# Kernel tuning notes

Measured on AMD Instinct MI355X. Metric: run time of the kernel, lower is better.

## Reference

```python
import jax, jax.numpy as jnp
import numpy as np
import math

# ---- module hyperparams (from init_kwargs) ----
L = 10            # number of hash-grid levels
DIM = 4           # features per level
LOG2T = 16
T = 1 << LOG2T    # hash table size per level
BASE = 16         # base resolution
PLS = 2.0         # per_level_scale
SCALE_MULTI = 0.5
HID = 64
IN_DIM = L * DIM  # 40
OUT_DIM = 13      # 1 + 12
N = 1_000_000

# growth factor b = exp((ln(finest) - ln(base)) / (L - 1)), finest = base * pls**L
B_GROWTH = math.exp((math.log(BASE * PLS ** L) - math.log(BASE)) / (L - 1))
RES = [int(math.floor(BASE * B_GROWTH ** l)) for l in range(L)]

PRIMES = np.array([1, 2654435761, 805459861], dtype=np.uint32)
# 8 corner offsets of a voxel
OFFS = np.array([[i, j, k] for i in (0, 1) for j in (0, 1) for k in (0, 1)], dtype=np.uint32)


def _hash_coords(c):
    # c: uint32 [N, 8, 3] -> int32 [N, 8] indices into table of size T
    p = jnp.asarray(PRIMES)
    h = (c[..., 0] * p[0]) ^ (c[..., 1] * p[1]) ^ (c[..., 2] * p[2])
    return (h & jnp.uint32(T - 1)).astype(jnp.int32)


def _encode(x, tables):
    # x: [N,3] in [0,1]; tables: [L, T, DIM] -> [N, DIM, L]
    offs_u = jnp.asarray(OFFS)                      # uint32 [8,3]
    offs_b = jnp.asarray(OFFS.astype(bool))         # bool   [8,3]
    feats = []
    for l in range(L):
        xs = x * RES[l]
        bottom = jnp.floor(xs)
        frac = xs - bottom                          # [N,3]
        corners = bottom.astype(jnp.uint32)[:, None, :] + offs_u[None]  # [N,8,3]
        idx = _hash_coords(corners)                 # [N,8]
        cf = tables[l][idx]                         # [N,8,DIM] gather
        # trilinear weights: prod over dims of frac (if offset==1) else (1-frac)
        w = jnp.prod(jnp.where(offs_b[None], frac[:, None, :], 1.0 - frac[:, None, :]), axis=-1)  # [N,8]
        feats.append(jnp.einsum('nc,ncd->nd', w, cf))  # [N,DIM]
    return jnp.stack(feats, axis=-1)                # [N, DIM, L]


def setup_inputs() -> dict:
    key = jax.random.key(0)
    ks = jax.random.split(key, 10)
    x = jax.random.uniform(ks[0], (N, 3), dtype=jnp.float32)
    cr = jax.random.uniform(ks[1], (N,), dtype=jnp.float32)
    tables = jax.random.uniform(ks[2], (L, T, DIM), dtype=jnp.float32, minval=-1e-4, maxval=1e-4)
    gain = math.sqrt(2.0)  # calculate_gain('relu')

    def xavier(k, fan_in, fan_out):
        a = gain * math.sqrt(6.0 / (fan_in + fan_out))
        return jax.random.uniform(k, (fan_in, fan_out), dtype=jnp.float32, minval=-a, maxval=a)

    W1 = xavier(ks[3], IN_DIM, HID)
    b1 = jnp.zeros((HID,), jnp.float32)
    W2 = xavier(ks[4], HID, HID)
    b2 = jnp.zeros((HID,), jnp.float32)
    W3 = xavier(ks[5], HID, OUT_DIM)
    b3 = jnp.zeros((OUT_DIM,), jnp.float32)
    return {"x": x, "cr": cr, "tables": tables,
            "W1": W1, "b1": b1, "W2": W2, "b2": b2, "W3": W3, "b3": b3}


def reference(x, cr, tables, W1, b1, W2, b2, W3, b3):
    enc = _encode(x, tables)                        # [N, DIM, L]
    cr_s = cr.reshape(-1) * SCALE_MULTI             # [N]
    n = jnp.arange(L, dtype=jnp.float32).reshape(1, 1, L)
    denom = PLS * 4.0 * n * cr_s[:, None, None]     # [N,1,L]
    erf_x = 1.0 / jnp.sqrt(jnp.maximum(denom, 1e-12))  # safe_div/safe_sqrt; erf(huge)=1 at n=0
    scaling = jax.lax.erf(erf_x)
    h = (enc * scaling).reshape(-1, IN_DIM)         # [N, 40]
    h = jax.nn.selu(h @ W1 + b1)
    h = jax.nn.selu(h @ W2 + b2)
    return h @ W3 + b3                              # [N, 13]
```

## Files before the change

### kernel.cpp

```cpp
#include <hip/hip_runtime.h>
#include <cmath>

typedef unsigned int uint32;
typedef __bf16 bf16;
typedef __bf16 bf16x8 __attribute__((ext_vector_type(8)));
typedef float f32x4 __attribute__((ext_vector_type(4)));

#define LVLS 10
#define TSIZE 65536
#define TMASK 65535u
#define PRIME2 2654435761u
#define PRIME3 805459861u

#define WOFF_W1 0
#define WOFF_W2 4096
#define WOFF_W3 8192
#define W_ELEMS 9216
#define DQ_OFF 18432
#define SC_OFF 18496
#define TAB_OFF_B 18560
#define TAB_ELEMS_F (LVLS * TSIZE * 4)
#define WS_NEEDED ((size_t)TAB_OFF_B + (size_t)TAB_ELEMS_F)

struct KParams { float resf[LVLS]; };

__global__ void scale_kernel(const float* __restrict__ tables, unsigned* __restrict__ scales) {
  int tid = blockIdx.x * 256 + threadIdx.x;
  int i4 = tid * 4;
  if (i4 >= TAB_ELEMS_F) return;
  float4 v = *(const float4*)(tables + i4);
  float m = fmaxf(fmaxf(fabsf(v.x), fabsf(v.y)), fmaxf(fabsf(v.z), fabsf(v.w)));
#pragma unroll
  for (int off = 32; off; off >>= 1) m = fmaxf(m, __shfl_xor(m, off, 64));
  if ((threadIdx.x & 63) == 0) {
    int l = i4 >> 18;
    atomicMax(scales + l, __float_as_uint(m));
  }
}

__global__ void quant_kernel(const float* __restrict__ W1, const float* __restrict__ W2,
                             const float* __restrict__ W3, const float* __restrict__ tables,
                             char* __restrict__ ws8, int do_tab) {
  int tid = blockIdx.x * 256 + threadIdx.x;
  bf16* wsb = (bf16*)ws8;
  if (tid < W_ELEMS) {
    float v;
    if (tid < 4096) {
      int n = tid >> 6, k = tid & 63;
      v = (k < 40) ? W1[k * 64 + n] : 0.f;
    } else if (tid < 8192) {
      int t2 = tid - 4096; int n = t2 >> 6, k = t2 & 63;
      v = W2[k * 64 + n];
    } else {
      int t3 = tid - 8192; int n = t3 >> 6, k = t3 & 63;
      v = (n < 13) ? W3[k * 13 + n] : 0.f;
    }
    wsb[tid] = (bf16)v;
  }
  const unsigned* scales = (const unsigned*)(ws8 + SC_OFF);
  if (tid < LVLS) {
    float s = __uint_as_float(scales[tid]);
    ((float*)(ws8 + DQ_OFF))[tid] = s * (1.0f / 127.0f);
  }
  if (do_tab) {
    int i4 = tid * 4;
    if (i4 < TAB_ELEMS_F) {
      float4 v = *(const float4*)(tables + i4);
      int l = i4 >> 18;
      float s = __uint_as_float(scales[l]);
      float r = (s > 0.f) ? 127.f / s : 0.f;
      int q0 = (int)rintf(fminf(fmaxf(v.x * r, -127.f), 127.f));
      int q1 = (int)rintf(fminf(fmaxf(v.y * r, -127.f), 127.f));
      int q2 = (int)rintf(fminf(fmaxf(v.z * r, -127.f), 127.f));
      int q3 = (int)rintf(fminf(fmaxf(v.w * r, -127.f), 127.f));
      unsigned p = (q0 & 0xff) | ((q1 & 0xff) << 8) | ((q2 & 0xff) << 16) | ((q3 & 0xff) << 24);
      *(unsigned*)(ws8 + TAB_OFF_B + i4) = p;
    }
  }
}

__device__ __forceinline__ float selu_f(float v) {
  float neg = 1.6732632423543772f * (__expf(v) - 1.0f);
  return 1.0507009873554805f * (v > 0.f ? v : neg);
}

__device__ __forceinline__ void gemm_stage(const bf16* __restrict__ Arow,
                                           const bf16* __restrict__ Bbase,
                                           const float* __restrict__ bvec,
                                           bf16* __restrict__ Hwr, int lr) {
  float bias[4];
#pragma unroll
  for (int nt = 0; nt < 4; ++nt) bias[nt] = bvec[nt * 16 + lr];
  f32x4 acc[4][4];
#pragma unroll
  for (int ms = 0; ms < 4; ++ms)
#pragma unroll
    for (int nt = 0; nt < 4; ++nt) {
      f32x4 a = {bias[nt], bias[nt], bias[nt], bias[nt]};
      acc[ms][nt] = a;
    }
  bf16x8 Bf[2][4];
#pragma unroll
  for (int ks = 0; ks < 2; ++ks)
#pragma unroll
    for (int nt = 0; nt < 4; ++nt)
      Bf[ks][nt] = *(const bf16x8*)(Bbase + nt * 1024 + ks * 32);
#pragma unroll
  for (int ks = 0; ks < 2; ++ks) {
    bf16x8 Af[4];
#pragma unroll
    for (int ms = 0; ms < 4; ++ms) Af[ms] = *(const bf16x8*)(Arow + ms * 1152 + ks * 32);
#pragma unroll
    for (int ms = 0; ms < 4; ++ms)
#pragma unroll
      for (int nt = 0; nt < 4; ++nt)
        acc[ms][nt] = __builtin_amdgcn_mfma_f32_16x16x32_bf16(Af[ms], Bf[ks][nt], acc[ms][nt], 0, 0, 0);
  }
#pragma unroll
  for (int ms = 0; ms < 4; ++ms)
#pragma unroll
    for (int nt = 0; nt < 4; ++nt)
#pragma unroll
      for (int r = 0; r < 4; ++r)
        Hwr[(ms * 16 + r) * 72 + nt * 16 + lr] = (bf16)selu_f(acc[ms][nt][r]);
}

template <bool TB>
__global__ __launch_bounds__(256, 4)
void ngp_fused(const float* __restrict__ x, const float* __restrict__ cr,
               const float* __restrict__ tables, const char* __restrict__ ws8,
               const float* __restrict__ b1, const float* __restrict__ b2,
               const float* __restrict__ b3, float* __restrict__ out,
               int N, KParams kp) {
  __shared__ bf16 Hbuf[256 * 72];
  const int tid = threadIdx.x;
  const int n = blockIdx.x * 256 + tid;
  const int ncl = (n < N) ? n : 0;

  const float px = x[ncl * 3 + 0];
  const float py = x[ncl * 3 + 1];
  const float pz = x[ncl * 3 + 2];
  const float crv = cr[ncl];
  const float* dq = (const float*)(ws8 + DQ_OFF);

  float feat[40];
#pragma unroll
  for (int l = 0; l < LVLS; ++l) {
    const float rs = kp.resf[l];
    float xs = px * rs, ys = py * rs, zs = pz * rs;
    float bx = floorf(xs), by = floorf(ys), bz = floorf(zs);
    float fx = xs - bx, fy = ys - by, fz = zs - bz;
    uint32 cx = (uint32)bx, cy = (uint32)by, cz = (uint32)bz;
    uint32 hx0 = cx, hx1 = cx + 1u;
    uint32 hy0 = cy * PRIME2, hy1 = hy0 + PRIME2;
    uint32 hz0 = cz * PRIME3, hz1 = hz0 + PRIME3;
    uint32 idx[8];
    idx[0] = (hx0 ^ hy0 ^ hz0) & TMASK; idx[1] = (hx0 ^ hy0 ^ hz1) & TMASK;
    idx[2] = (hx0 ^ hy1 ^ hz0) & TMASK; idx[3] = (hx0 ^ hy1 ^ hz1) & TMASK;
    idx[4] = (hx1 ^ hy0 ^ hz0) & TMASK; idx[5] = (hx1 ^ hy0 ^ hz1) & TMASK;
    idx[6] = (hx1 ^ hy1 ^ hz0) & TMASK; idx[7] = (hx1 ^ hy1 ^ hz1) & TMASK;

    float f[8][4];
    if (TB) {
      const unsigned* tb = ((const unsigned*)(ws8 + TAB_OFF_B)) + l * TSIZE;
#pragma unroll
      for (int c = 0; c < 8; ++c) {
        unsigned q = tb[idx[c]];
        f[c][0] = (float)(signed char)(q & 0xff);
        f[c][1] = (float)(signed char)((q >> 8) & 0xff);
        f[c][2] = (float)(signed char)((q >> 16) & 0xff);
        f[c][3] = (float)(signed char)(q >> 24);
      }
    } else {
      const float4* tb = ((const float4*)tables) + l * TSIZE;
#pragma unroll
      for (int c = 0; c < 8; ++c) {
        float4 q = tb[idx[c]];
        f[c][0] = q.x; f[c][1] = q.y; f[c][2] = q.z; f[c][3] = q.w;
      }
    }
    float wx1 = fx, wx0 = 1.f - fx, wy1 = fy, wy0 = 1.f - fy, wz1 = fz, wz0 = 1.f - fz;
    float wxy00 = wx0 * wy0, wxy01 = wx0 * wy1, wxy10 = wx1 * wy0, wxy11 = wx1 * wy1;
    float w[8] = {wxy00 * wz0, wxy00 * wz1, wxy01 * wz0, wxy01 * wz1,
                  wxy10 * wz0, wxy10 * wz1, wxy11 * wz0, wxy11 * wz1};
    float a0 = 0.f, a1 = 0.f, a2 = 0.f, a3 = 0.f;
#pragma unroll
    for (int c = 0; c < 8; ++c) {
      a0 = fmaf(w[c], f[c][0], a0);
      a1 = fmaf(w[c], f[c][1], a1);
      a2 = fmaf(w[c], f[c][2], a2);
      a3 = fmaf(w[c], f[c][3], a3);
    }
    float s = erff(rsqrtf(fmaxf(4.0f * (float)l * crv, 1e-12f)));
    if (TB) s *= dq[l];
    feat[0 * 10 + l] = a0 * s;
    feat[1 * 10 + l] = a1 * s;
    feat[2 * 10 + l] = a2 * s;
    feat[3 * 10 + l] = a3 * s;
  }

  {
    bf16* row = Hbuf + tid * 72;
#pragma unroll
    for (int c = 0; c < 5; ++c) {
      bf16x8 v;
#pragma unroll
      for (int j = 0; j < 8; ++j) v[j] = (bf16)feat[c * 8 + j];
      *(bf16x8*)(row + c * 8) = v;
    }
    bf16x8 z;
#pragma unroll
    for (int j = 0; j < 8; ++j) z[j] = (bf16)0.f;
    *(bf16x8*)(row + 40) = z;
    *(bf16x8*)(row + 48) = z;
    *(bf16x8*)(row + 56) = z;
  }
  __syncthreads();

  const int w = tid >> 6;
  const int lane = tid & 63;
  const int lr = lane & 15;
  const int quad = lane >> 4;
  const bf16* wsb = (const bf16*)ws8;

  const bf16* Arow = Hbuf + (w * 64 + lr) * 72 + quad * 8;
  bf16* Hwr = Hbuf + (w * 64 + quad * 4) * 72;

  gemm_stage(Arow, wsb + WOFF_W1 + lr * 64 + quad * 8, b1, Hwr, lr);
  __syncthreads();
  gemm_stage(Arow, wsb + WOFF_W2 + lr * 64 + quad * 8, b2, Hwr, lr);
  __syncthreads();

  {
    float b3v = (lr < 13) ? b3[lr] : 0.f;
    f32x4 acc3[4];
#pragma unroll
    for (int ms = 0; ms < 4; ++ms) {
      f32x4 a = {b3v, b3v, b3v, b3v};
      acc3[ms] = a;
    }
    const bf16* B3b = wsb + WOFF_W3 + lr * 64 + quad * 8;
    bf16x8 B3[2];
    B3[0] = *(const bf16x8*)(B3b);
    B3[1] = *(const bf16x8*)(B3b + 32);
#pragma unroll
    for (int ks = 0; ks < 2; ++ks) {
      bf16x8 Af[4];
#pragma unroll
      for (int ms = 0; ms < 4; ++ms) Af[ms] = *(const bf16x8*)(Arow + ms * 1152 + ks * 32);
#pragma unroll
      for (int ms = 0; ms < 4; ++ms)
        acc3[ms] = __builtin_amdgcn_mfma_f32_16x16x32_bf16(Af[ms], B3[ks], acc3[ms], 0, 0, 0);
    }
    const int rbase = blockIdx.x * 256 + w * 64 + quad * 4;
#pragma unroll
    for (int ms = 0; ms < 4; ++ms)
#pragma unroll
      for (int r = 0; r < 4; ++r) {
        int rowg = rbase + ms * 16 + r;
        if (lr < 13 && rowg < N) out[rowg * 13 + lr] = acc3[ms][r];
      }
  }
}

extern "C" void kernel_launch(void* const* d_in, const int* in_sizes, int n_in,
                              void* d_out, int out_size, void* d_ws, size_t ws_size,
                              hipStream_t stream) {
  const float* x      = (const float*)d_in[0];
  const float* cr     = (const float*)d_in[1];
  const float* tables = (const float*)d_in[2];
  const float* W1     = (const float*)d_in[3];
  const float* b1     = (const float*)d_in[4];
  const float* W2     = (const float*)d_in[5];
  const float* b2     = (const float*)d_in[6];
  const float* W3     = (const float*)d_in[7];
  const float* b3     = (const float*)d_in[8];
  float* out = (float*)d_out;
  const int N = in_sizes[1];

  KParams kp;
  double B = exp((log(16.0 * pow(2.0, 10.0)) - log(16.0)) / 9.0);
  for (int l = 0; l < LVLS; ++l) kp.resf[l] = (float)floor(16.0 * pow(B, (double)l));

  char* ws8 = (char*)d_ws;
  const bool tb = ws_size >= WS_NEEDED;

  const int qblocks = (TAB_ELEMS_F / 4 + 255) / 256;
  if (tb) {
    hipMemsetAsync(ws8 + SC_OFF, 0, 64, stream);
    scale_kernel<<<qblocks, 256, 0, stream>>>(tables, (unsigned*)(ws8 + SC_OFF));
    quant_kernel<<<qblocks, 256, 0, stream>>>(W1, W2, W3, tables, ws8, 1);
  } else {
    quant_kernel<<<(W_ELEMS + 255) / 256, 256, 0, stream>>>(W1, W2, W3, tables, ws8, 0);
  }

  int blocks = (N + 255) / 256;
  if (tb)
    ngp_fused<true><<<blocks, 256, 0, stream>>>(x, cr, tables, ws8, b1, b2, b3, out, N, kp);
  else
    ngp_fused<false><<<blocks, 256, 0, stream>>>(x, cr, tables, ws8, b1, b2, b3, out, N, kp);
}
```

Measured before the change: 485.1 us.

## Swizzle LDS activations, prefetch next-level gathers, stage output for coalesced stores

Several changes land together. The LDS activation buffer drops its 72-element padded rows for a 64-element XOR-swizzled layout, and the GEMM stage now loads all A fragments once and processes the N-tiles in two halves to cut register pressure. Launch bounds go from 4 to 5 waves per SIMD. The int8 table path is software-pipelined: level l+1 gathers are issued before level l is consumed. Table values are stored with a +128 offset so unpacking is a plain unsigned convert, with the offset subtracted after accumulation, and level-0 erf is skipped. Output rows are staged in LDS and written as coalesced float4 stores. The risks are more live registers from the prefetch under the tighter launch bound, and extra barriers.

```diff
diff --git a/kernel.cpp b/kernel.cpp
--- a/kernel.cpp
+++ b/kernel.cpp
@@ -69,10 +69,10 @@
       int l = i4 >> 18;
       float s = __uint_as_float(scales[l]);
       float r = (s > 0.f) ? 127.f / s : 0.f;
-      int q0 = (int)rintf(fminf(fmaxf(v.x * r, -127.f), 127.f));
-      int q1 = (int)rintf(fminf(fmaxf(v.y * r, -127.f), 127.f));
-      int q2 = (int)rintf(fminf(fmaxf(v.z * r, -127.f), 127.f));
-      int q3 = (int)rintf(fminf(fmaxf(v.w * r, -127.f), 127.f));
+      int q0 = (int)rintf(fminf(fmaxf(v.x * r, -127.f), 127.f)) + 128;
+      int q1 = (int)rintf(fminf(fmaxf(v.y * r, -127.f), 127.f)) + 128;
+      int q2 = (int)rintf(fminf(fmaxf(v.z * r, -127.f), 127.f)) + 128;
+      int q3 = (int)rintf(fminf(fmaxf(v.w * r, -127.f), 127.f)) + 128;
       unsigned p = (q0 & 0xff) | ((q1 & 0xff) << 8) | ((q2 & 0xff) << 16) | ((q3 & 0xff) << 24);
       *(unsigned*)(ws8 + TAB_OFF_B + i4) = p;
     }
@@ -84,55 +84,82 @@
   return 1.0507009873554805f * (v > 0.f ? v : neg);
 }
 
-__device__ __forceinline__ void gemm_stage(const bf16* __restrict__ Arow,
+__device__ __forceinline__ bf16* hswz(bf16* Hb, int row, int cb) {
+  return (bf16*)((char*)Hb + (row << 7) + (cb ^ ((row & 7) << 4)));
+}
+
+__device__ __forceinline__ void gemm_stage(bf16* __restrict__ Hb, int w, int lr, int quad,
                                            const bf16* __restrict__ Bbase,
-                                           const float* __restrict__ bvec,
-                                           bf16* __restrict__ Hwr, int lr) {
-  float bias[4];
-#pragma unroll
-  for (int nt = 0; nt < 4; ++nt) bias[nt] = bvec[nt * 16 + lr];
-  f32x4 acc[4][4];
-#pragma unroll
-  for (int ms = 0; ms < 4; ++ms)
-#pragma unroll
-    for (int nt = 0; nt < 4; ++nt) {
-      f32x4 a = {bias[nt], bias[nt], bias[nt], bias[nt]};
-      acc[ms][nt] = a;
-    }
-  bf16x8 Bf[2][4];
+                                           const float* __restrict__ bvec) {
+  bf16x8 Af[2][4];
 #pragma unroll
   for (int ks = 0; ks < 2; ++ks)
 #pragma unroll
-    for (int nt = 0; nt < 4; ++nt)
-      Bf[ks][nt] = *(const bf16x8*)(Bbase + nt * 1024 + ks * 32);
-#pragma unroll
-  for (int ks = 0; ks < 2; ++ks) {
-    bf16x8 Af[4];
-#pragma unroll
-    for (int ms = 0; ms < 4; ++ms) Af[ms] = *(const bf16x8*)(Arow + ms * 1152 + ks * 32);
-#pragma unroll
     for (int ms = 0; ms < 4; ++ms)
-#pragma unroll
-      for (int nt = 0; nt < 4; ++nt)
-        acc[ms][nt] = __builtin_amdgcn_mfma_f32_16x16x32_bf16(Af[ms], Bf[ks][nt], acc[ms][nt], 0, 0, 0);
-  }
-#pragma unroll
-  for (int ms = 0; ms < 4; ++ms)
-#pragma unroll
-    for (int nt = 0; nt < 4; ++nt)
-#pragma unroll
-      for (int r = 0; r < 4; ++r)
-        Hwr[(ms * 16 + r) * 72 + nt * 16 + lr] = (bf16)selu_f(acc[ms][nt][r]);
-}
+      Af[ks][ms] = *(const bf16x8*)hswz(Hb, w * 64 + ms * 16 + lr, quad * 16 + ks * 64);
+#pragma unroll
+  for (int h = 0; h < 2; ++h) {
+    f32x4 acc[4][2];
+#pragma unroll
+    for (int nt2 = 0; nt2 < 2; ++nt2) {
+      float b = bvec[(h * 2 + nt2) * 16 + lr];
+#pragma unroll
+      for (int ms = 0; ms < 4; ++ms) {
+        f32x4 a = {b, b, b, b};
+        acc[ms][nt2] = a;
+      }
+    }
+#pragma unroll
+    for (int ks = 0; ks < 2; ++ks) {
+      bf16x8 B0 = *(const bf16x8*)(Bbase + (h * 2 + 0) * 1024 + ks * 32);
+      bf16x8 B1 = *(const bf16x8*)(Bbase + (h * 2 + 1) * 1024 + ks * 32);
+#pragma unroll
+      for (int ms = 0; ms < 4; ++ms) {
+        acc[ms][0] = __builtin_amdgcn_mfma_f32_16x16x32_bf16(Af[ks][ms], B0, acc[ms][0], 0, 0, 0);
+        acc[ms][1] = __builtin_amdgcn_mfma_f32_16x16x32_bf16(Af[ks][ms], B1, acc[ms][1], 0, 0, 0);
+      }
+    }
+#pragma unroll
+    for (int ms = 0; ms < 4; ++ms)
+#pragma unroll
+      for (int nt2 = 0; nt2 < 2; ++nt2)
+#pragma unroll
+        for (int r = 0; r < 4; ++r) {
+          int row = w * 64 + quad * 4 + ms * 16 + r;
+          *hswz(Hb, row, ((h * 2 + nt2) * 16 + lr) * 2) = (bf16)selu_f(acc[ms][nt2][r]);
+        }
+  }
+}
+
+#define CALC_IDX(L, IDX, F0, F1, F2)                                   \
+  do {                                                                 \
+    const float rs_ = kp.resf[(L)];                                    \
+    float xs_ = px * rs_, ys_ = py * rs_, zs_ = pz * rs_;              \
+    float bx_ = floorf(xs_), by_ = floorf(ys_), bz_ = floorf(zs_);     \
+    (F0) = xs_ - bx_; (F1) = ys_ - by_; (F2) = zs_ - bz_;              \
+    uint32 cx_ = (uint32)bx_, cy_ = (uint32)by_, cz_ = (uint32)bz_;    \
+    uint32 hy0_ = cy_ * PRIME2, hy1_ = hy0_ + PRIME2;                  \
+    uint32 hz0_ = cz_ * PRIME3, hz1_ = hz0_ + PRIME3;                  \
+    uint32 cx1_ = cx_ + 1u;                                            \
+    uint32 bse_ = (uint32)(L) << 16;                                   \
+    (IDX)[0] = ((cx_ ^ hy0_ ^ hz0_) & TMASK) | bse_;                   \
+    (IDX)[1] = ((cx_ ^ hy0_ ^ hz1_) & TMASK) | bse_;                   \
+    (IDX)[2] = ((cx_ ^ hy1_ ^ hz0_) & TMASK) | bse_;                   \
+    (IDX)[3] = ((cx_ ^ hy1_ ^ hz1_) & TMASK) | bse_;                   \
+    (IDX)[4] = ((cx1_ ^ hy0_ ^ hz0_) & TMASK) | bse_;                  \
+    (IDX)[5] = ((cx1_ ^ hy0_ ^ hz1_) & TMASK) | bse_;                  \
+    (IDX)[6] = ((cx1_ ^ hy1_ ^ hz0_) & TMASK) | bse_;                  \
+    (IDX)[7] = ((cx1_ ^ hy1_ ^ hz1_) & TMASK) | bse_;                  \
+  } while (0)
 
 template <bool TB>
-__global__ __launch_bounds__(256, 4)
+__global__ __launch_bounds__(256, 5)
 void ngp_fused(const float* __restrict__ x, const float* __restrict__ cr,
                const float* __restrict__ tables, const char* __restrict__ ws8,
                const float* __restrict__ b1, const float* __restrict__ b2,
                const float* __restrict__ b3, float* __restrict__ out,
                int N, KParams kp) {
-  __shared__ bf16 Hbuf[256 * 72];
+  __shared__ __align__(16) bf16 Hbuf[256 * 64];
   const int tid = threadIdx.x;
   const int n = blockIdx.x * 256 + tid;
   const int ncl = (n < N) ? n : 0;
@@ -144,76 +171,102 @@
   const float* dq = (const float*)(ws8 + DQ_OFF);
 
   float feat[40];
-#pragma unroll
-  for (int l = 0; l < LVLS; ++l) {
-    const float rs = kp.resf[l];
-    float xs = px * rs, ys = py * rs, zs = pz * rs;
-    float bx = floorf(xs), by = floorf(ys), bz = floorf(zs);
-    float fx = xs - bx, fy = ys - by, fz = zs - bz;
-    uint32 cx = (uint32)bx, cy = (uint32)by, cz = (uint32)bz;
-    uint32 hx0 = cx, hx1 = cx + 1u;
-    uint32 hy0 = cy * PRIME2, hy1 = hy0 + PRIME2;
-    uint32 hz0 = cz * PRIME3, hz1 = hz0 + PRIME3;
-    uint32 idx[8];
-    idx[0] = (hx0 ^ hy0 ^ hz0) & TMASK; idx[1] = (hx0 ^ hy0 ^ hz1) & TMASK;
-    idx[2] = (hx0 ^ hy1 ^ hz0) & TMASK; idx[3] = (hx0 ^ hy1 ^ hz1) & TMASK;
-    idx[4] = (hx1 ^ hy0 ^ hz0) & TMASK; idx[5] = (hx1 ^ hy0 ^ hz1) & TMASK;
-    idx[6] = (hx1 ^ hy1 ^ hz0) & TMASK; idx[7] = (hx1 ^ hy1 ^ hz1) & TMASK;
-
-    float f[8][4];
-    if (TB) {
-      const unsigned* tb = ((const unsigned*)(ws8 + TAB_OFF_B)) + l * TSIZE;
+
+  if constexpr (TB) {
+    const unsigned* tb = (const unsigned*)(ws8 + TAB_OFF_B);
+    uint32 idx0[8];
+    float pf0, pf1, pf2;
+    CALC_IDX(0, idx0, pf0, pf1, pf2);
+    unsigned qP[8];
+#pragma unroll
+    for (int c = 0; c < 8; ++c) qP[c] = tb[idx0[c]];
+#pragma unroll
+    for (int l = 0; l < LVLS; ++l) {
+      unsigned qN[8];
+      float nf0 = 0.f, nf1 = 0.f, nf2 = 0.f;
+      if (l + 1 < LVLS) {
+        uint32 idxN[8];
+        CALC_IDX(l + 1, idxN, nf0, nf1, nf2);
+#pragma unroll
+        for (int c = 0; c < 8; ++c) qN[c] = tb[idxN[c]];
+      }
+      float fx = pf0, fy = pf1, fz = pf2;
+      float wx1 = fx, wx0 = 1.f - fx, wy1 = fy, wy0 = 1.f - fy, wz1 = fz, wz0 = 1.f - fz;
+      float wxy00 = wx0 * wy0, wxy01 = wx0 * wy1, wxy10 = wx1 * wy0, wxy11 = wx1 * wy1;
+      float w8[8] = {wxy00 * wz0, wxy00 * wz1, wxy01 * wz0, wxy01 * wz1,
+                     wxy10 * wz0, wxy10 * wz1, wxy11 * wz0, wxy11 * wz1};
+      float a0 = 0.f, a1 = 0.f, a2 = 0.f, a3 = 0.f;
 #pragma unroll
       for (int c = 0; c < 8; ++c) {
-        unsigned q = tb[idx[c]];
-        f[c][0] = (float)(signed char)(q & 0xff);
-        f[c][1] = (float)(signed char)((q >> 8) & 0xff);
-        f[c][2] = (float)(signed char)((q >> 16) & 0xff);
-        f[c][3] = (float)(signed char)(q >> 24);
-      }
-    } else {
-      const float4* tb = ((const float4*)tables) + l * TSIZE;
+        unsigned q = qP[c];
+        float u0 = (float)(q & 0xffu);
+        float u1 = (float)((q >> 8) & 0xffu);
+        float u2 = (float)((q >> 16) & 0xffu);
+        float u3 = (float)(q >> 24);
+        a0 = fmaf(w8[c], u0, a0);
+        a1 = fmaf(w8[c], u1, a1);
+        a2 = fmaf(w8[c], u2, a2);
+        a3 = fmaf(w8[c], u3, a3);
+      }
+      float s = (l == 0) ? dq[0]
+                         : erff(rsqrtf(fmaxf(4.0f * (float)l * crv, 1e-12f))) * dq[l];
+      feat[0 * 10 + l] = (a0 - 128.f) * s;
+      feat[1 * 10 + l] = (a1 - 128.f) * s;
+      feat[2 * 10 + l] = (a2 - 128.f) * s;
+      feat[3 * 10 + l] = (a3 - 128.f) * s;
+      if (l + 1 < LVLS) {
+#pragma unroll
+        for (int c = 0; c < 8; ++c) qP[c] = qN[c];
+        pf0 = nf0; pf1 = nf1; pf2 = nf2;
+      }
+    }
+  } else {
+#pragma unroll
+    for (int l = 0; l < LVLS; ++l) {
+      uint32 idx[8];
+      float fx, fy, fz;
+      CALC_IDX(l, idx, fx, fy, fz);
+      const float4* tb4 = (const float4*)tables;
+      float f[8][4];
 #pragma unroll
       for (int c = 0; c < 8; ++c) {
-        float4 q = tb[idx[c]];
+        float4 q = tb4[idx[c]];
         f[c][0] = q.x; f[c][1] = q.y; f[c][2] = q.z; f[c][3] = q.w;
       }
-    }
-    float wx1 = fx, wx0 = 1.f - fx, wy1 = fy, wy0 = 1.f - fy, wz1 = fz, wz0 = 1.f - fz;
-    float wxy00 = wx0 * wy0, wxy01 = wx0 * wy1, wxy10 = wx1 * wy0, wxy11 = wx1 * wy1;
-    float w[8] = {wxy00 * wz0, wxy00 * wz1, wxy01 * wz0, wxy01 * wz1,
-                  wxy10 * wz0, wxy10 * wz1, wxy11 * wz0, wxy11 * wz1};
-    float a0 = 0.f, a1 = 0.f, a2 = 0.f, a3 = 0.f;
-#pragma unroll
-    for (int c = 0; c < 8; ++c) {
-      a0 = fmaf(w[c], f[c][0], a0);
-      a1 = fmaf(w[c], f[c][1], a1);
-      a2 = fmaf(w[c], f[c][2], a2);
-      a3 = fmaf(w[c], f[c][3], a3);
-    }
-    float s = erff(rsqrtf(fmaxf(4.0f * (float)l * crv, 1e-12f)));
-    if (TB) s *= dq[l];
-    feat[0 * 10 + l] = a0 * s;
-    feat[1 * 10 + l] = a1 * s;
-    feat[2 * 10 + l] = a2 * s;
-    feat[3 * 10 + l] = a3 * s;
+      float wx1 = fx, wx0 = 1.f - fx, wy1 = fy, wy0 = 1.f - fy, wz1 = fz, wz0 = 1.f - fz;
+      float wxy00 = wx0 * wy0, wxy01 = wx0 * wy1, wxy10 = wx1 * wy0, wxy11 = wx1 * wy1;
+      float w8[8] = {wxy00 * wz0, wxy00 * wz1, wxy01 * wz0, wxy01 * wz1,
+                     wxy10 * wz0, wxy10 * wz1, wxy11 * wz0, wxy11 * wz1};
+      float a0 = 0.f, a1 = 0.f, a2 = 0.f, a3 = 0.f;
+#pragma unroll
+      for (int c = 0; c < 8; ++c) {
+        a0 = fmaf(w8[c], f[c][0], a0);
+        a1 = fmaf(w8[c], f[c][1], a1);
+        a2 = fmaf(w8[c], f[c][2], a2);
+        a3 = fmaf(w8[c], f[c][3], a3);
+      }
+      float s = (l == 0) ? 1.0f : erff(rsqrtf(fmaxf(4.0f * (float)l * crv, 1e-12f)));
+      feat[0 * 10 + l] = a0 * s;
+      feat[1 * 10 + l] = a1 * s;
+      feat[2 * 10 + l] = a2 * s;
+      feat[3 * 10 + l] = a3 * s;
+    }
   }
 
   {
-    bf16* row = Hbuf + tid * 72;
 #pragma unroll
     for (int c = 0; c < 5; ++c) {
       bf16x8 v;
 #pragma unroll
       for (int j = 0; j < 8; ++j) v[j] = (bf16)feat[c * 8 + j];
-      *(bf16x8*)(row + c * 8) = v;
+      *(bf16x8*)hswz(Hbuf, tid, c * 16) = v;
     }
     bf16x8 z;
 #pragma unroll
     for (int j = 0; j < 8; ++j) z[j] = (bf16)0.f;
-    *(bf16x8*)(row + 40) = z;
-    *(bf16x8*)(row + 48) = z;
-    *(bf16x8*)(row + 56) = z;
+    *(bf16x8*)hswz(Hbuf, tid, 80) = z;
+    *(bf16x8*)hswz(Hbuf, tid, 96) = z;
+    *(bf16x8*)hswz(Hbuf, tid, 112) = z;
   }
   __syncthreads();
 
@@ -223,12 +276,9 @@
   const int quad = lane >> 4;
   const bf16* wsb = (const bf16*)ws8;
 
-  const bf16* Arow = Hbuf + (w * 64 + lr) * 72 + quad * 8;
-  bf16* Hwr = Hbuf + (w * 64 + quad * 4) * 72;
-
-  gemm_stage(Arow, wsb + WOFF_W1 + lr * 64 + quad * 8, b1, Hwr, lr);
+  gemm_stage(Hbuf, w, lr, quad, wsb + WOFF_W1 + lr * 64 + quad * 8, b1);
   __syncthreads();
-  gemm_stage(Arow, wsb + WOFF_W2 + lr * 64 + quad * 8, b2, Hwr, lr);
+  gemm_stage(Hbuf, w, lr, quad, wsb + WOFF_W2 + lr * 64 + quad * 8, b2);
   __syncthreads();
 
   {
@@ -247,19 +297,37 @@
     for (int ks = 0; ks < 2; ++ks) {
       bf16x8 Af[4];
 #pragma unroll
-      for (int ms = 0; ms < 4; ++ms) Af[ms] = *(const bf16x8*)(Arow + ms * 1152 + ks * 32);
+      for (int ms = 0; ms < 4; ++ms)
+        Af[ms] = *(const bf16x8*)hswz(Hbuf, w * 64 + ms * 16 + lr, quad * 16 + ks * 64);
 #pragma unroll
       for (int ms = 0; ms < 4; ++ms)
         acc3[ms] = __builtin_amdgcn_mfma_f32_16x16x32_bf16(Af[ms], B3[ks], acc3[ms], 0, 0, 0);
     }
-    const int rbase = blockIdx.x * 256 + w * 64 + quad * 4;
+    __syncthreads();
+    float* Obuf = (float*)Hbuf;
 #pragma unroll
     for (int ms = 0; ms < 4; ++ms)
 #pragma unroll
-      for (int r = 0; r < 4; ++r) {
-        int rowg = rbase + ms * 16 + r;
-        if (lr < 13 && rowg < N) out[rowg * 13 + lr] = acc3[ms][r];
-      }
+      for (int r = 0; r < 4; ++r)
+        if (lr < 13)
+          Obuf[(w * 64 + quad * 4 + ms * 16 + r) * 13 + lr] = acc3[ms][r];
+    __syncthreads();
+
+    const int base = blockIdx.x * 256;
+    int nrows = N - base;
+    if (nrows >= 256) {
+      float4* og4 = (float4*)(out + (size_t)base * 13);
+      const float4* Ob4 = (const float4*)Obuf;
+#pragma unroll
+      for (int i = 0; i < 4; ++i) {
+        int j = tid + i * 256;
+        if (j < 832) og4[j] = Ob4[j];
+      }
+    } else {
+      const int nfl = nrows * 13;
+      float* og = out + (size_t)base * 13;
+      for (int j = tid; j < nfl; j += 256) og[j] = Obuf[j];
+    }
   }
 }
 
```

After: 639.7 us. 31.9% more time.
